# Optimization experiments

Hardware: AMD Instinct MI355X
Metric: run time of the kernel (lower is better)

Reference implementation:

```python
import jax, jax.numpy as jnp
import numpy as np

N_NODES = 10000
N_EDGES = 50000
NUM_GENES = 1000
HEADS = 8
DIMS_IN = [256, 448 * 8, 384 * 8, 256 * 8]
DIMS_OUT = [448, 384, 256, NUM_GENES]
HEADS_L = [8, 8, 8, 1]


def _leaky_relu(x):
    return jnp.where(x >= 0, x, 0.2 * x)


def gat_conv(x, src, dst, n, W, a_src, a_dst, b, heads, c):
    # W: [heads*c, f_in]; a_src/a_dst: [heads, c]; b: [heads*c]
    h = (x @ W.T).reshape(n, heads, c)                      # [N,H,C]
    al_s = jnp.einsum('nhc,hc->nh', h, a_src)               # [N,H]
    al_d = jnp.einsum('nhc,hc->nh', h, a_dst)
    e = _leaky_relu(al_s[src] + al_d[dst])                  # [E,H]
    # segment softmax over incoming edges of each dst node
    m = jax.ops.segment_max(e, dst, num_segments=n)
    e = jnp.exp(e - m[dst])
    s = jax.ops.segment_sum(e, dst, num_segments=n)
    alpha = e / (s[dst] + 1e-16)
    out = jax.ops.segment_sum(h[src] * alpha[:, :, None], dst, num_segments=n)
    return out.reshape(n, heads * c) + b


def graph_ln(x, w, b):
    # PyG LayerNorm mode='graph': normalize over all node features of the graph
    mu = x.mean()
    var = ((x - mu) ** 2).mean()
    return (x - mu) * jax.lax.rsqrt(var + 1e-5) * w + b


def setup_inputs() -> dict:
    key = jax.random.key(0)
    ks = jax.random.split(key, 32)
    inp = {
        'x': jax.random.normal(ks[0], (N_NODES, DIMS_IN[0]), dtype=jnp.float32),
        'edge_index': jax.random.randint(ks[1], (2, N_EDGES), 0, N_NODES, dtype=jnp.int32),
    }
    ki = 2
    for li in range(4):
        h, c, fin = HEADS_L[li], DIMS_OUT[li], DIMS_IN[li]
        inp[f'W{li+1}'] = jax.random.normal(ks[ki], (h * c, fin), dtype=jnp.float32) * (fin ** -0.5); ki += 1
        inp[f'a_src{li+1}'] = jax.random.normal(ks[ki], (h, c), dtype=jnp.float32) * 0.1; ki += 1
        inp[f'a_dst{li+1}'] = jax.random.normal(ks[ki], (h, c), dtype=jnp.float32) * 0.1; ki += 1
        inp[f'b{li+1}'] = jnp.zeros((h * c,), dtype=jnp.float32)
        if li < 3:
            inp[f'ln{li+1}_w'] = jnp.ones((h * c,), dtype=jnp.float32)
            inp[f'ln{li+1}_b'] = jnp.zeros((h * c,), dtype=jnp.float32)
    return inp


def reference(x, edge_index,
              W1, a_src1, a_dst1, b1, ln1_w, ln1_b,
              W2, a_src2, a_dst2, b2, ln2_w, ln2_b,
              W3, a_src3, a_dst3, b3, ln3_w, ln3_b,
              W4, a_src4, a_dst4, b4):
    n = x.shape[0]
    loops = jnp.arange(n, dtype=edge_index.dtype)
    src = jnp.concatenate([edge_index[0], loops])  # add_self_loops=True (PyG default)
    dst = jnp.concatenate([edge_index[1], loops])
    h = jax.nn.relu(gat_conv(x, src, dst, n, W1, a_src1, a_dst1, b1, 8, 448))
    h = graph_ln(h, ln1_w, ln1_b)
    h = jax.nn.relu(gat_conv(h, src, dst, n, W2, a_src2, a_dst2, b2, 8, 384))
    h = graph_ln(h, ln2_w, ln2_b)
    h = jax.nn.relu(gat_conv(h, src, dst, n, W3, a_src3, a_dst3, b3, 8, 256))
    h = graph_ln(h, ln3_w, ln3_b)
    out = gat_conv(h, src, dst, n, W4, a_src4, a_dst4, b4, 1, NUM_GENES)
    return out
```

## Files before the change

kernel.cpp:

```cpp
#include <hip/hip_runtime.h>

typedef _Float16 h8 __attribute__((ext_vector_type(8)));
typedef _Float16 h4 __attribute__((ext_vector_type(4)));
typedef __attribute__((ext_vector_type(4))) float facc4;

__device__ __forceinline__ void gload16(const void* g, void* l) {
  __builtin_amdgcn_global_load_lds((const __attribute__((address_space(1))) void*)g,
                                   (__attribute__((address_space(3))) void*)l, 16, 0, 0);
}

__global__ void f2h_k(const float* __restrict__ in, unsigned short* __restrict__ out, int n4) {
  int i = blockIdx.x * 256 + threadIdx.x;
  int stride = gridDim.x * 256;
  for (; i < n4; i += stride) {
    float4 v = ((const float4*)in)[i];
    h4 o;
    o[0] = (_Float16)v.x; o[1] = (_Float16)v.y; o[2] = (_Float16)v.z; o[3] = (_Float16)v.w;
    ((h4*)out)[i] = o;
  }
}

__global__ __launch_bounds__(512, 2) void gemm_f16(
    const unsigned short* __restrict__ A, const unsigned short* __restrict__ B,
    unsigned short* __restrict__ Hout,
    float* __restrict__ als, float* __restrict__ ald,
    const float* __restrict__ a_src, const float* __restrict__ a_dst,
    int M, int Nn, int K, int C, int H, int gx, int nwg) {
  __shared__ __align__(16) unsigned short lds[3 * 16384];
  const int tid = threadIdx.x, lane = tid & 63, wv = tid >> 6;

  int lin = blockIdx.x;
  int q = nwg >> 3, r = nwg & 7;
  int xcd = lin & 7, idx = lin >> 3;
  int swz = (xcd < r) ? (xcd * (q + 1) + idx) : (r * (q + 1) + (xcd - r) * q + idx);
  const int bx = swz % gx, by = swz / gx;
  const int brow = by * 256, bcol = bx * 256;
  const int wr = wv >> 2, wc = wv & 3;

  const int l4 = lane >> 2;
  const int srcslot = ((lane & 3) ^ ((lane >> 3) & 3)) * 8;
  int ar0 = brow + wv * 16 + l4;        if (ar0 > M - 1)  ar0 = M - 1;
  int ar1 = brow + wv * 16 + 128 + l4;  if (ar1 > M - 1)  ar1 = M - 1;
  int br0 = bcol + wv * 16 + l4;        if (br0 > Nn - 1) br0 = Nn - 1;
  int br1 = bcol + wv * 16 + 128 + l4;  if (br1 > Nn - 1) br1 = Nn - 1;
  const unsigned short* pa0 = A + (size_t)ar0 * K + srcslot;
  const unsigned short* pa1 = A + (size_t)ar1 * K + srcslot;
  const unsigned short* pb0 = B + (size_t)br0 * K + srcslot;
  const unsigned short* pb1 = B + (size_t)br1 * K + srcslot;
  const int d0 = wv * 512, d1 = wv * 512 + 4096;

  const int rsl = ((lane >> 4) ^ (((lane & 15) >> 1) & 3)) * 8;
  const int baseA = (wr * 128 + (lane & 15)) * 32 + rsl;
  const int baseB = 8192 + (wc * 64 + (lane & 15)) * 32 + rsl;

  facc4 acc[8][4] = {};
  const int nt = K >> 5;

  auto STAGE = [&](int kt, int buf) {
    unsigned short* Lq = &lds[buf * 16384];
    const int kb = kt * 32;
    gload16(pa0 + kb, Lq + d0);
    gload16(pa1 + kb, Lq + d1);
    gload16(pb0 + kb, Lq + 8192 + d0);
    gload16(pb1 + kb, Lq + 8192 + d1);
  };

  STAGE(0, 0);
  STAGE(1, 1);
  asm volatile("s_waitcnt vmcnt(4)" ::: "memory");
  __builtin_amdgcn_s_barrier();
  asm volatile("" ::: "memory");

  int cb = 0, sb = 2;
  for (int kt = 0; kt < nt; ++kt) {
    if (kt + 2 < nt) STAGE(kt + 2, sb);
    const unsigned short* Lq = &lds[cb * 16384];
    h8 af[8], bf[4];
#pragma unroll
    for (int m = 0; m < 8; ++m) af[m] = *(const h8*)(Lq + baseA + m * 512);
#pragma unroll
    for (int n = 0; n < 4; ++n) bf[n] = *(const h8*)(Lq + baseB + n * 512);
    __builtin_amdgcn_s_setprio(1);
#pragma unroll
    for (int m = 0; m < 8; ++m)
#pragma unroll
      for (int n = 0; n < 4; ++n)
        acc[m][n] = __builtin_amdgcn_mfma_f32_16x16x32_f16(af[m], bf[n], acc[m][n], 0, 0, 0);
    __builtin_amdgcn_s_setprio(0);
    if (kt + 2 < nt) asm volatile("s_waitcnt vmcnt(4)" ::: "memory");
    else             asm volatile("s_waitcnt vmcnt(0)" ::: "memory");
    __builtin_amdgcn_s_barrier();
    asm volatile("" ::: "memory");
    cb = (cb == 2) ? 0 : cb + 1;
    sb = (sb == 2) ? 0 : sb + 1;
  }

  const int rbase = brow + wr * 128 + ((lane >> 4) << 2);
  const int cbase = bcol + wc * 64 + (lane & 15);

  float asv[4], adv[4];
#pragma unroll
  for (int n = 0; n < 4; ++n) {
    int col = cbase + n * 16;
    bool ok = col < Nn;
    asv[n] = ok ? a_src[col] : 0.f;
    adv[n] = ok ? a_dst[col] : 0.f;
  }
  const int hh = (bcol + wc * 64) / C;
#pragma unroll
  for (int m = 0; m < 8; ++m)
#pragma unroll
    for (int r2 = 0; r2 < 4; ++r2) {
      float s1 = 0.f, s2 = 0.f;
#pragma unroll
      for (int n = 0; n < 4; ++n) { float v = acc[m][n][r2]; s1 += v * asv[n]; s2 += v * adv[n]; }
#pragma unroll
      for (int mm = 1; mm < 16; mm <<= 1) { s1 += __shfl_xor(s1, mm); s2 += __shfl_xor(s2, mm); }
      int row = rbase + m * 16 + r2;
      if ((lane & 15) == 0 && row < M) {
        atomicAdd(&als[row * H + hh], s1);
        atomicAdd(&ald[row * H + hh], s2);
      }
    }

#pragma unroll
  for (int m = 0; m < 8; ++m)
#pragma unroll
    for (int n = 0; n < 4; ++n) {
      int col = cbase + n * 16;
      if (col >= Nn) continue;
#pragma unroll
      for (int r2 = 0; r2 < 4; ++r2) {
        int row = rbase + m * 16 + r2;
        if (row < M) {
          _Float16 hv = (_Float16)acc[m][n][r2];
          Hout[(size_t)row * Nn + col] = *(unsigned short*)&hv;
        }
      }
    }
}

__global__ __launch_bounds__(512, 2) void gemm_f16_hd(
    const unsigned short* __restrict__ Aall, const unsigned short* __restrict__ Ball,
    unsigned short* __restrict__ Xout, const float* __restrict__ bias,
    float* __restrict__ lnsums, int M, int K, int Fo, int Ch, int gx, int nwg) {
  __shared__ __align__(16) unsigned short lds[3 * 16384];
  const int tid = threadIdx.x, lane = tid & 63, wv = tid >> 6;
  const int head = blockIdx.y;
  const unsigned short* A = Aall + (size_t)head * M * K;
  const unsigned short* B = Ball + (size_t)head * Ch * K;

  int lin = blockIdx.x;
  int q = nwg >> 3, r = nwg & 7;
  int xcd = lin & 7, idx = lin >> 3;
  int swz = (xcd < r) ? (xcd * (q + 1) + idx) : (r * (q + 1) + (xcd - r) * q + idx);
  const int bx = swz % gx, by = swz / gx;
  const int brow = by * 256, bcol = bx * 256;
  const int wr = wv >> 2, wc = wv & 3;

  const int l4 = lane >> 2;
  const int srcslot = ((lane & 3) ^ ((lane >> 3) & 3)) * 8;
  int ar0 = brow + wv * 16 + l4;        if (ar0 > M - 1)  ar0 = M - 1;
  int ar1 = brow + wv * 16 + 128 + l4;  if (ar1 > M - 1)  ar1 = M - 1;
  int br0 = bcol + wv * 16 + l4;        if (br0 > Ch - 1) br0 = Ch - 1;
  int br1 = bcol + wv * 16 + 128 + l4;  if (br1 > Ch - 1) br1 = Ch - 1;
  const unsigned short* pa0 = A + (size_t)ar0 * K + srcslot;
  const unsigned short* pa1 = A + (size_t)ar1 * K + srcslot;
  const unsigned short* pb0 = B + (size_t)br0 * K + srcslot;
  const unsigned short* pb1 = B + (size_t)br1 * K + srcslot;
  const int d0 = wv * 512, d1 = wv * 512 + 4096;

  const int rsl = ((lane >> 4) ^ (((lane & 15) >> 1) & 3)) * 8;
  const int baseA = (wr * 128 + (lane & 15)) * 32 + rsl;
  const int baseB = 8192 + (wc * 64 + (lane & 15)) * 32 + rsl;

  facc4 acc[8][4] = {};
  const int nt = K >> 5;

  auto STAGE = [&](int kt, int buf) {
    unsigned short* Lq = &lds[buf * 16384];
    const int kb = kt * 32;
    gload16(pa0 + kb, Lq + d0);
    gload16(pa1 + kb, Lq + d1);
    gload16(pb0 + kb, Lq + 8192 + d0);
    gload16(pb1 + kb, Lq + 8192 + d1);
  };

  STAGE(0, 0);
  STAGE(1, 1);
  asm volatile("s_waitcnt vmcnt(4)" ::: "memory");
  __builtin_amdgcn_s_barrier();
  asm volatile("" ::: "memory");

  int cb = 0, sb = 2;
  for (int kt = 0; kt < nt; ++kt) {
    if (kt + 2 < nt) STAGE(kt + 2, sb);
    const unsigned short* Lq = &lds[cb * 16384];
    h8 af[8], bf[4];
#pragma unroll
    for (int m = 0; m < 8; ++m) af[m] = *(const h8*)(Lq + baseA + m * 512);
#pragma unroll
    for (int n = 0; n < 4; ++n) bf[n] = *(const h8*)(Lq + baseB + n * 512);
    __builtin_amdgcn_s_setprio(1);
#pragma unroll
    for (int m = 0; m < 8; ++m)
#pragma unroll
      for (int n = 0; n < 4; ++n)
        acc[m][n] = __builtin_amdgcn_mfma_f32_16x16x32_f16(af[m], bf[n], acc[m][n], 0, 0, 0);
    __builtin_amdgcn_s_setprio(0);
    if (kt + 2 < nt) asm volatile("s_waitcnt vmcnt(4)" ::: "memory");
    else             asm volatile("s_waitcnt vmcnt(0)" ::: "memory");
    __builtin_amdgcn_s_barrier();
    asm volatile("" ::: "memory");
    cb = (cb == 2) ? 0 : cb + 1;
    sb = (sb == 2) ? 0 : sb + 1;
  }

  const int rbase = brow + wr * 128 + ((lane >> 4) << 2);
  const int cbase = bcol + wc * 64 + (lane & 15);
  float s1 = 0.f, s2 = 0.f;
#pragma unroll
  for (int n = 0; n < 4; ++n) {
    int col_l = cbase + n * 16;
    if (col_l >= Ch) continue;
    int col_g = head * Ch + col_l;
    float bv = bias[col_g];
#pragma unroll
    for (int m = 0; m < 8; ++m)
#pragma unroll
      for (int r2 = 0; r2 < 4; ++r2) {
        int row = rbase + m * 16 + r2;
        if (row < M) {
          float v = acc[m][n][r2] + bv;
          _Float16 hv = (_Float16)v;
          Xout[(size_t)row * Fo + col_g] = *(unsigned short*)&hv;
          float rv = v > 0.f ? v : 0.f;
          s1 += rv; s2 += rv * rv;
        }
      }
  }
#pragma unroll
  for (int m = 32; m; m >>= 1) { s1 += __shfl_down(s1, m); s2 += __shfl_down(s2, m); }
  __shared__ float r1s[8], r2s[8];
  if (lane == 0) { r1s[wv] = s1; r2s[wv] = s2; }
  __syncthreads();
  if (tid == 0) {
    float t1 = 0.f, t2 = 0.f;
#pragma unroll
    for (int w = 0; w < 8; ++w) { t1 += r1s[w]; t2 += r2s[w]; }
    atomicAdd(&lnsums[0], t1);
    atomicAdd(&lnsums[1], t2);
  }
}

__global__ void attw_k(const float* __restrict__ W, const float* __restrict__ as_,
                       const float* __restrict__ ad_, float* __restrict__ ws,
                       float* __restrict__ wd, int C, int K) {
  int t = blockIdx.x * 256 + threadIdx.x;
  int h = t / K, k = t % K;
  float s1 = 0.f, s2 = 0.f;
  for (int c = 0; c < C; ++c) {
    float w = W[(size_t)(h * C + c) * K + k];
    s1 += as_[h * C + c] * w;
    s2 += ad_[h * C + c] * w;
  }
  ws[t] = s1; wd[t] = s2;
}

__global__ __launch_bounds__(256) void logits_x_k(
    const float* __restrict__ x, const float* __restrict__ ws, const float* __restrict__ wd,
    float* __restrict__ als, float* __restrict__ ald, int n) {
  __shared__ float sws[2048], swd[2048];
  for (int i = threadIdx.x; i < 2048; i += 256) { sws[i] = ws[i]; swd[i] = wd[i]; }
  __syncthreads();
  int node = blockIdx.x * 4 + (threadIdx.x >> 6);
  int lane = threadIdx.x & 63;
  if (node >= n) return;
  const float* xp = x + (size_t)node * 256;
  float s1[8] = {}, s2[8] = {};
  for (int k = lane; k < 256; k += 64) {
    float xv = xp[k];
#pragma unroll
    for (int h = 0; h < 8; ++h) { s1[h] += xv * sws[h * 256 + k]; s2[h] += xv * swd[h * 256 + k]; }
  }
#pragma unroll
  for (int m = 32; m; m >>= 1)
#pragma unroll
    for (int h = 0; h < 8; ++h) { s1[h] += __shfl_down(s1[h], m); s2[h] += __shfl_down(s2[h], m); }
  if (lane == 0) {
#pragma unroll
    for (int h = 0; h < 8; ++h) { als[node * 8 + h] = s1[h]; ald[node * 8 + h] = s2[h]; }
  }
}

__global__ __launch_bounds__(256) void aggregate_x_k(
    const unsigned short* __restrict__ x16,
    const float* __restrict__ als, const float* __restrict__ ald,
    const int* __restrict__ rowptr, const int* __restrict__ esrc,
    unsigned short* __restrict__ aggx, int n) {
  const int node = blockIdx.x, tid = threadIdx.x;
  int beg = rowptr[node];
  int deg = rowptr[node + 1] - beg;
  if (deg > 64) deg = 64;
  __shared__ int   s_src[64];
  __shared__ float s_al[64][8];
  __shared__ float s_inv[8];
  __shared__ unsigned short s_x[64][256];
  float aldv[8];
#pragma unroll
  for (int h = 0; h < 8; ++h) aldv[h] = ald[node * 8 + h];
  for (int d = tid; d < deg; d += 256) {
    int s = esrc[beg + d];
    s_src[d] = s;
#pragma unroll
    for (int h = 0; h < 8; ++h) {
      float v = als[s * 8 + h] + aldv[h];
      s_al[d][h] = (v >= 0.f) ? v : 0.2f * v;
    }
  }
  __syncthreads();
  if (tid < 8) {
    float m = -1e30f;
    for (int d = 0; d < deg; ++d) m = fmaxf(m, s_al[d][tid]);
    float s = 0.f;
    for (int d = 0; d < deg; ++d) { float p = __expf(s_al[d][tid] - m); s_al[d][tid] = p; s += p; }
    s_inv[tid] = 1.f / (s + 1e-16f);
  }
  for (int c = tid; c < deg * 32; c += 256) {
    int d = c >> 5, q = c & 31;
    ((h8*)s_x[d])[q] = ((const h8*)(x16 + (size_t)s_src[d] * 256))[q];
  }
  __syncthreads();
  const int h = tid >> 5, k8 = tid & 31;
  float a[8] = {};
  for (int d = 0; d < deg; ++d) {
    float al = s_al[d][h] * s_inv[h];
    h8 xv = ((const h8*)s_x[d])[k8];
#pragma unroll
    for (int j = 0; j < 8; ++j) a[j] = fmaf(al, (float)xv[j], a[j]);
  }
  h8 o;
#pragma unroll
  for (int j = 0; j < 8; ++j) o[j] = (_Float16)a[j];
  *(h8*)(aggx + ((size_t)h * n + node) * 256 + k8 * 8) = o;
}

__global__ void count_deg_k(const int* __restrict__ ei, int* __restrict__ deg, int Ereal, int Etot) {
  int e = blockIdx.x * 256 + threadIdx.x;
  if (e >= Etot) return;
  int dst = (e < Ereal) ? ei[Ereal + e] : (e - Ereal);
  atomicAdd(&deg[dst], 1);
}

__global__ void scan_k(const int* __restrict__ deg, int* __restrict__ rowptr, int n) {
  __shared__ int sums[1024];
  int t = threadIdx.x;
  int base = t * 10;
  int loc[10]; int s = 0;
#pragma unroll
  for (int i = 0; i < 10; ++i) { int idx = base + i; int d = (idx < n) ? deg[idx] : 0; loc[i] = s; s += d; }
  sums[t] = s;
  __syncthreads();
  for (int off = 1; off < 1024; off <<= 1) {
    int add = (t >= off) ? sums[t - off] : 0;
    __syncthreads();
    sums[t] += add;
    __syncthreads();
  }
  int excl = sums[t] - s;
#pragma unroll
  for (int i = 0; i < 10; ++i) { int idx = base + i; if (idx < n) rowptr[idx] = excl + loc[i]; }
  if (t == 1023) rowptr[n] = sums[1023];
}

__global__ void scatter_k(const int* __restrict__ ei, const int* __restrict__ rowptr,
                          int* __restrict__ fill, int* __restrict__ esrc,
                          int Ereal, int Etot) {
  int e = blockIdx.x * 256 + threadIdx.x;
  if (e >= Etot) return;
  int src = (e < Ereal) ? ei[e] : (e - Ereal);
  int dst = (e < Ereal) ? ei[Ereal + e] : (e - Ereal);
  int pos = rowptr[dst] + atomicAdd(&fill[dst], 1);
  esrc[pos] = src;
}

template <int H, bool FP32OUT, bool STATS>
__global__ __launch_bounds__(256) void aggregate_k(
    const unsigned short* __restrict__ hfp,
    const float* __restrict__ als, const float* __restrict__ ald,
    const int* __restrict__ rowptr, const int* __restrict__ esrc,
    const float* __restrict__ bias, void* __restrict__ outv,
    float* __restrict__ lnsums, int C, int F) {
  const int node = blockIdx.x;
  const int tid = threadIdx.x;
  int beg = rowptr[node];
  int deg = rowptr[node + 1] - beg;
  if (deg > 128) deg = 128;
  __shared__ int   s_src[128];
  __shared__ float s_p[128][H];
  __shared__ float s_inv[H];
  float aldv[H];
#pragma unroll
  for (int h = 0; h < H; ++h) aldv[h] = ald[node * H + h];
  for (int d = tid; d < deg; d += 256) {
    int s = esrc[beg + d];
    s_src[d] = s;
#pragma unroll
    for (int h = 0; h < H; ++h) {
      float v = als[s * H + h] + aldv[h];
      s_p[d][h] = (v >= 0.f) ? v : 0.2f * v;
    }
  }
  __syncthreads();
  if (tid < H) {
    float m = -1e30f;
    for (int d = 0; d < deg; ++d) m = fmaxf(m, s_p[d][tid]);
    float s = 0.f;
    for (int d = 0; d < deg; ++d) { float p = __expf(s_p[d][tid] - m); s_p[d][tid] = p; s += p; }
    s_inv[tid] = 1.f / (s + 1e-16f);
  }
  __syncthreads();

  float s1 = 0.f, s2 = 0.f;
  const int F8 = F >> 3;
  for (int c8 = tid; c8 < F8; c8 += 256) {
    int f0 = c8 * 8;
    int h = f0 / C;
    float a[8];
    float4 b0 = *(const float4*)(bias + f0);
    float4 b1 = *(const float4*)(bias + f0 + 4);
    a[0] = b0.x; a[1] = b0.y; a[2] = b0.z; a[3] = b0.w;
    a[4] = b1.x; a[5] = b1.y; a[6] = b1.z; a[7] = b1.w;
    for (int d = 0; d < deg; ++d) {
      float al = s_p[d][h] * s_inv[h];
      h8 hv = *(const h8*)(hfp + (size_t)s_src[d] * F + f0);
#pragma unroll
      for (int j = 0; j < 8; ++j) a[j] = fmaf(al, (float)hv[j], a[j]);
    }
    size_t i = (size_t)node * F + f0;
    if (FP32OUT) {
      float4 o0 = {a[0], a[1], a[2], a[3]};
      float4 o1 = {a[4], a[5], a[6], a[7]};
      *(float4*)((float*)outv + i) = o0;
      *(float4*)((float*)outv + i + 4) = o1;
    } else {
      h8 o;
#pragma unroll
      for (int j = 0; j < 8; ++j) o[j] = (_Float16)a[j];
      *(h8*)((unsigned short*)outv + i) = o;
    }
    if (STATS) {
#pragma unroll
      for (int j = 0; j < 8; ++j) { float v = a[j] > 0.f ? a[j] : 0.f; s1 += v; s2 += v * v; }
    }
  }
  if (STATS) {
#pragma unroll
    for (int m = 32; m; m >>= 1) { s1 += __shfl_down(s1, m); s2 += __shfl_down(s2, m); }
    __shared__ float r1[4], r2[4];
    if ((tid & 63) == 0) { r1[tid >> 6] = s1; r2[tid >> 6] = s2; }
    __syncthreads();
    if (tid == 0) {
      atomicAdd(&lnsums[0], r1[0] + r1[1] + r1[2] + r1[3]);
      atomicAdd(&lnsums[1], r2[0] + r2[1] + r2[2] + r2[3]);
    }
  }
}

__global__ void ln_apply_k(unsigned short* __restrict__ x, const float* __restrict__ sums,
                           const float* __restrict__ w, const float* __restrict__ b,
                           int total8, int F8, float inv_count) {
  int i8 = blockIdx.x * 256 + threadIdx.x;
  if (i8 >= total8) return;
  float mu = sums[0] * inv_count;
  float var = sums[1] * inv_count - mu * mu;
  float istd = rsqrtf(var + 1e-5f);
  int f0 = (i8 % F8) * 8;
  h8 hv = *(h8*)(x + (size_t)i8 * 8);
  float4 w0 = *(const float4*)(w + f0), w1 = *(const float4*)(w + f0 + 4);
  float4 b0 = *(const float4*)(b + f0), b1 = *(const float4*)(b + f0 + 4);
  float wv[8] = {w0.x, w0.y, w0.z, w0.w, w1.x, w1.y, w1.z, w1.w};
  float bv[8] = {b0.x, b0.y, b0.z, b0.w, b1.x, b1.y, b1.z, b1.w};
  h8 o;
#pragma unroll
  for (int j = 0; j < 8; ++j) {
    float v = (float)hv[j]; v = v > 0.f ? v : 0.f;
    o[j] = (_Float16)((v - mu) * istd * wv[j] + bv[j]);
  }
  *(h8*)(x + (size_t)i8 * 8) = o;
}

extern "C" void kernel_launch(void* const* d_in, const int* in_sizes, int n_in,
                              void* d_out, int out_size, void* d_ws, size_t ws_size,
                              hipStream_t stream) {
  const int N = 10000, Ereal = 50000, Etot = 60000;
  const float* x  = (const float*)d_in[0];
  const int*   ei = (const int*)d_in[1];
  const float* W[4]    = {(const float*)d_in[2],  (const float*)d_in[8],  (const float*)d_in[14], (const float*)d_in[20]};
  const float* asrc[4] = {(const float*)d_in[3],  (const float*)d_in[9],  (const float*)d_in[15], (const float*)d_in[21]};
  const float* adst[4] = {(const float*)d_in[4],  (const float*)d_in[10], (const float*)d_in[16], (const float*)d_in[22]};
  const float* bias[4] = {(const float*)d_in[5],  (const float*)d_in[11], (const float*)d_in[17], (const float*)d_in[23]};
  const float* lnw[3]  = {(const float*)d_in[6],  (const float*)d_in[12], (const float*)d_in[18]};
  const float* lnb[3]  = {(const float*)d_in[7],  (const float*)d_in[13], (const float*)d_in[19]};

  const int fin[4]  = {256, 3584, 3072, 2048};
  const int fout[4] = {3584, 3072, 2048, 1000};
  const int CH[4]   = {448, 384, 256, 1000};

  size_t off = 0;
  char* base = (char*)d_ws;
  auto alloc = [&](size_t bytes) -> void* {
    void* p = base + off;
    off += (bytes + 255) & ~(size_t)255;
    return p;
  };
  unsigned short* xh  = (unsigned short*)alloc((size_t)N * 3584 * 2);
  unsigned short* hh  = (unsigned short*)alloc((size_t)N * 3584 * 2);
  unsigned short* wh  = (unsigned short*)alloc((size_t)3072 * 3584 * 2);
  float*          alsA   = (float*)alloc((size_t)4 * N * 8 * 4);
  float*          aldA   = (float*)alloc((size_t)4 * N * 8 * 4);
  int*            deg    = (int*)alloc((size_t)N * 4);
  int*            fill   = (int*)alloc((size_t)N * 4);
  int*            rowptr = (int*)alloc((size_t)(N + 1) * 4);
  int*            esrc   = (int*)alloc((size_t)Etot * 4);
  float*          lnsums = (float*)alloc(256);
  float*          wsrc   = (float*)alloc((size_t)8 * 256 * 4);
  float*          wdst   = (float*)alloc((size_t)8 * 256 * 4);

  auto cdiv = [](int a, int b) { return (a + b - 1) / b; };

  hipMemsetAsync(deg, 0, (size_t)N * 4, stream);
  hipMemsetAsync(fill, 0, (size_t)N * 4, stream);
  hipMemsetAsync(alsA, 0, (size_t)4 * N * 8 * 4 * 2, stream);
  count_deg_k<<<cdiv(Etot, 256), 256, 0, stream>>>(ei, deg, Ereal, Etot);
  scan_k<<<1, 1024, 0, stream>>>(deg, rowptr, N);
  scatter_k<<<cdiv(Etot, 256), 256, 0, stream>>>(ei, rowptr, fill, esrc, Ereal, Etot);

  {
    int n4 = (N * fin[0]) / 4;
    f2h_k<<<min(2048, cdiv(n4, 256)), 256, 0, stream>>>(x, xh, n4);
  }

  {
    float* als = alsA;
    float* ald = aldA;
    attw_k<<<8, 256, 0, stream>>>(W[0], asrc[0], adst[0], wsrc, wdst, 448, 256);
    logits_x_k<<<cdiv(N, 4), 256, 0, stream>>>(x, wsrc, wdst, als, ald, N);
    {
      int n4 = (3584 * 256) / 4;
      f2h_k<<<min(2048, cdiv(n4, 256)), 256, 0, stream>>>(W[0], wh, n4);
    }
    aggregate_x_k<<<N, 256, 0, stream>>>(xh, als, ald, rowptr, esrc, hh, N);
    hipMemsetAsync(lnsums, 0, 8, stream);
    gemm_f16_hd<<<dim3(80, 8), 512, 0, stream>>>(hh, wh, xh, bias[0], lnsums,
                                                 N, 256, 3584, 448, 2, 80);
    int F8 = 3584 >> 3;
    ln_apply_k<<<cdiv(N * F8, 256), 256, 0, stream>>>(xh, lnsums, lnw[0], lnb[0],
                                                      N * F8, F8, 1.0f / (float)(N * 3584));
  }

  for (int l = 1; l < 4; ++l) {
    const int K = fin[l], Fo = fout[l], C = CH[l];
    const int H = (l == 3) ? 1 : 8;
    float* als = alsA + (size_t)l * N * 8;
    float* ald = aldA + (size_t)l * N * 8;

    {
      int n4 = (Fo * K) / 4;
      f2h_k<<<min(2048, cdiv(n4, 256)), 256, 0, stream>>>(W[l], wh, n4);
    }

    {
      int gx = cdiv(Fo, 256), gy = cdiv(N, 256);
      int nwg = gx * gy;
      gemm_f16<<<nwg, 512, 0, stream>>>(xh, wh, hh, als, ald, asrc[l], adst[l],
                                        N, Fo, K, C, H, gx, nwg);
    }

    if (l < 3) {
      hipMemsetAsync(lnsums, 0, 8, stream);
      aggregate_k<8, false, true><<<N, 256, 0, stream>>>(hh, als, ald, rowptr, esrc,
                                                         bias[l], xh, lnsums, C, Fo);
      int F8 = Fo >> 3;
      int total8 = N * F8;
      ln_apply_k<<<cdiv(total8, 256), 256, 0, stream>>>(xh, lnsums, lnw[l], lnb[l],
                                                        total8, F8, 1.0f / (float)(N * Fo));
    } else {
      aggregate_k<1, true, false><<<N, 256, 0, stream>>>(hh, als, ald, rowptr, esrc,
                                                         bias[l], d_out, nullptr, C, Fo);
    }
  }
}
```

Before: 1.504 ms.

## Fold graph LayerNorm into next layer's weights and drop ln_apply passes

Removes the separate ln_apply kernels. The activation is now stored post-ReLU, and the LayerNorm scale (istd*w) is folded into the fp16 weight conversion, with a per-output constant (W·(b - mu*istd*w)) computed in the same kernel and added to the GEMM accumulator. This saves a full read-modify-write pass over the large N×F activation per layer, plus some memsets. In exchange, the weight-conversion kernel does more per-element work and a reduction, and scaling the weights before fp16 rounding changes numerics, since the activation is no longer centred before the matmul.

```diff
diff --git a/kernel.cpp b/kernel.cpp
--- a/kernel.cpp
+++ b/kernel.cpp
@@ -20,11 +20,42 @@
   }
 }
 
+__global__ __launch_bounds__(256) void w2h_fold_k(
+    const float* __restrict__ W, const float* __restrict__ lnw, const float* __restrict__ lnb,
+    const float* __restrict__ sums, float inv_count,
+    unsigned short* __restrict__ wh, float* __restrict__ cvec, int K) {
+  const int o = blockIdx.x, tid = threadIdx.x;
+  float mu = sums[0] * inv_count;
+  float var = sums[1] * inv_count - mu * mu;
+  float istd = rsqrtf(var + 1e-5f);
+  const float* wrow = W + (size_t)o * K;
+  float dot = 0.f;
+  for (int k4 = tid; k4 < (K >> 2); k4 += 256) {
+    float4 wv = ((const float4*)wrow)[k4];
+    float4 gw = ((const float4*)lnw)[k4];
+    float4 gb = ((const float4*)lnb)[k4];
+    float sx = istd * gw.x, sy = istd * gw.y, sz = istd * gw.z, sw = istd * gw.w;
+    h4 oq;
+    oq[0] = (_Float16)(wv.x * sx); oq[1] = (_Float16)(wv.y * sy);
+    oq[2] = (_Float16)(wv.z * sz); oq[3] = (_Float16)(wv.w * sw);
+    ((h4*)(wh + (size_t)o * K))[k4] = oq;
+    dot += wv.x * (gb.x - mu * sx) + wv.y * (gb.y - mu * sy)
+         + wv.z * (gb.z - mu * sz) + wv.w * (gb.w - mu * sw);
+  }
+#pragma unroll
+  for (int m = 32; m; m >>= 1) dot += __shfl_down(dot, m);
+  __shared__ float r[4];
+  if ((tid & 63) == 0) r[tid >> 6] = dot;
+  __syncthreads();
+  if (tid == 0) cvec[o] = r[0] + r[1] + r[2] + r[3];
+}
+
 __global__ __launch_bounds__(512, 2) void gemm_f16(
     const unsigned short* __restrict__ A, const unsigned short* __restrict__ B,
     unsigned short* __restrict__ Hout,
     float* __restrict__ als, float* __restrict__ ald,
     const float* __restrict__ a_src, const float* __restrict__ a_dst,
+    const float* __restrict__ cvec,
     int M, int Nn, int K, int C, int H, int gx, int nwg) {
   __shared__ __align__(16) unsigned short lds[3 * 16384];
   const int tid = threadIdx.x, lane = tid & 63, wv = tid >> 6;
@@ -98,6 +129,16 @@
   const int rbase = brow + wr * 128 + ((lane >> 4) << 2);
   const int cbase = bcol + wc * 64 + (lane & 15);
 
+#pragma unroll
+  for (int n = 0; n < 4; ++n) {
+    int col = cbase + n * 16;
+    float cadd = (col < Nn) ? cvec[col] : 0.f;
+#pragma unroll
+    for (int m = 0; m < 8; ++m)
+#pragma unroll
+      for (int r2 = 0; r2 < 4; ++r2) acc[m][n][r2] += cadd;
+  }
+
   float asv[4], adv[4];
 #pragma unroll
   for (int n = 0; n < 4; ++n) {
@@ -232,9 +273,9 @@
         int row = rbase + m * 16 + r2;
         if (row < M) {
           float v = acc[m][n][r2] + bv;
-          _Float16 hv = (_Float16)v;
+          float rv = v > 0.f ? v : 0.f;
+          _Float16 hv = (_Float16)rv;
           Xout[(size_t)row * Fo + col_g] = *(unsigned short*)&hv;
-          float rv = v > 0.f ? v : 0.f;
           s1 += rv; s2 += rv * rv;
         }
       }
@@ -327,8 +368,8 @@
     s_inv[tid] = 1.f / (s + 1e-16f);
   }
   for (int c = tid; c < deg * 32; c += 256) {
-    int d = c >> 5, q = c & 31;
-    ((h8*)s_x[d])[q] = ((const h8*)(x16 + (size_t)s_src[d] * 256))[q];
+    int d = c >> 5, q2 = c & 31;
+    ((h8*)s_x[d])[q2] = ((const h8*)(x16 + (size_t)s_src[d] * 256))[q2];
   }
   __syncthreads();
   const int h = tid >> 5, k8 = tid & 31;
@@ -437,6 +478,10 @@
 #pragma unroll
       for (int j = 0; j < 8; ++j) a[j] = fmaf(al, (float)hv[j], a[j]);
     }
+    if (STATS) {
+#pragma unroll
+      for (int j = 0; j < 8; ++j) { float v = a[j] > 0.f ? a[j] : 0.f; a[j] = v; s1 += v; s2 += v * v; }
+    }
     size_t i = (size_t)node * F + f0;
     if (FP32OUT) {
       float4 o0 = {a[0], a[1], a[2], a[3]};
@@ -449,10 +494,6 @@
       for (int j = 0; j < 8; ++j) o[j] = (_Float16)a[j];
       *(h8*)((unsigned short*)outv + i) = o;
     }
-    if (STATS) {
-#pragma unroll
-      for (int j = 0; j < 8; ++j) { float v = a[j] > 0.f ? a[j] : 0.f; s1 += v; s2 += v * v; }
-    }
   }
   if (STATS) {
 #pragma unroll
@@ -465,29 +506,6 @@
       atomicAdd(&lnsums[1], r2[0] + r2[1] + r2[2] + r2[3]);
     }
   }
-}
-
-__global__ void ln_apply_k(unsigned short* __restrict__ x, const float* __restrict__ sums,
-                           const float* __restrict__ w, const float* __restrict__ b,
-                           int total8, int F8, float inv_count) {
-  int i8 = blockIdx.x * 256 + threadIdx.x;
-  if (i8 >= total8) return;
-  float mu = sums[0] * inv_count;
-  float var = sums[1] * inv_count - mu * mu;
-  float istd = rsqrtf(var + 1e-5f);
-  int f0 = (i8 % F8) * 8;
-  h8 hv = *(h8*)(x + (size_t)i8 * 8);
-  float4 w0 = *(const float4*)(w + f0), w1 = *(const float4*)(w + f0 + 4);
-  float4 b0 = *(const float4*)(b + f0), b1 = *(const float4*)(b + f0 + 4);
-  float wv[8] = {w0.x, w0.y, w0.z, w0.w, w1.x, w1.y, w1.z, w1.w};
-  float bv[8] = {b0.x, b0.y, b0.z, b0.w, b1.x, b1.y, b1.z, b1.w};
-  h8 o;
-#pragma unroll
-  for (int j = 0; j < 8; ++j) {
-    float v = (float)hv[j]; v = v > 0.f ? v : 0.f;
-    o[j] = (_Float16)((v - mu) * istd * wv[j] + bv[j]);
-  }
-  *(h8*)(x + (size_t)i8 * 8) = o;
 }
 
 extern "C" void kernel_launch(void* const* d_in, const int* in_sizes, int n_in,
@@ -519,19 +537,20 @@
   unsigned short* wh  = (unsigned short*)alloc((size_t)3072 * 3584 * 2);
   float*          alsA   = (float*)alloc((size_t)4 * N * 8 * 4);
   float*          aldA   = (float*)alloc((size_t)4 * N * 8 * 4);
+  float*          lnsA   = (float*)alloc(256);
   int*            deg    = (int*)alloc((size_t)N * 4);
   int*            fill   = (int*)alloc((size_t)N * 4);
   int*            rowptr = (int*)alloc((size_t)(N + 1) * 4);
   int*            esrc   = (int*)alloc((size_t)Etot * 4);
-  float*          lnsums = (float*)alloc(256);
   float*          wsrc   = (float*)alloc((size_t)8 * 256 * 4);
   float*          wdst   = (float*)alloc((size_t)8 * 256 * 4);
+  float*          cvec   = (float*)alloc((size_t)3072 * 4);
 
   auto cdiv = [](int a, int b) { return (a + b - 1) / b; };
 
   hipMemsetAsync(deg, 0, (size_t)N * 4, stream);
   hipMemsetAsync(fill, 0, (size_t)N * 4, stream);
-  hipMemsetAsync(alsA, 0, (size_t)4 * N * 8 * 4 * 2, stream);
+  hipMemsetAsync(alsA, 0, (size_t)4 * N * 8 * 4 * 2 + 256, stream);
   count_deg_k<<<cdiv(Etot, 256), 256, 0, stream>>>(ei, deg, Ereal, Etot);
   scan_k<<<1, 1024, 0, stream>>>(deg, rowptr, N);
   scatter_k<<<cdiv(Etot, 256), 256, 0, stream>>>(ei, rowptr, fill, esrc, Ereal, Etot);
@@ -551,12 +570,8 @@
       f2h_k<<<min(2048, cdiv(n4, 256)), 256, 0, stream>>>(W[0], wh, n4);
     }
     aggregate_x_k<<<N, 256, 0, stream>>>(xh, als, ald, rowptr, esrc, hh, N);
-    hipMemsetAsync(lnsums, 0, 8, stream);
-    gemm_f16_hd<<<dim3(80, 8), 512, 0, stream>>>(hh, wh, xh, bias[0], lnsums,
+    gemm_f16_hd<<<dim3(80, 8), 512, 0, stream>>>(hh, wh, xh, bias[0], lnsA,
                                                  N, 256, 3584, 448, 2, 80);
-    int F8 = 3584 >> 3;
-    ln_apply_k<<<cdiv(N * F8, 256), 256, 0, stream>>>(xh, lnsums, lnw[0], lnb[0],
-                                                      N * F8, F8, 1.0f / (float)(N * 3584));
   }
 
   for (int l = 1; l < 4; ++l) {
@@ -565,26 +580,19 @@
     float* als = alsA + (size_t)l * N * 8;
     float* ald = aldA + (size_t)l * N * 8;
 
-    {
-      int n4 = (Fo * K) / 4;
-      f2h_k<<<min(2048, cdiv(n4, 256)), 256, 0, stream>>>(W[l], wh, n4);
-    }
+    w2h_fold_k<<<Fo, 256, 0, stream>>>(W[l], lnw[l - 1], lnb[l - 1], lnsA + (l - 1) * 2,
+                                       1.0f / (float)(N * fin[l]), wh, cvec, K);
 
     {
       int gx = cdiv(Fo, 256), gy = cdiv(N, 256);
       int nwg = gx * gy;
-      gemm_f16<<<nwg, 512, 0, stream>>>(xh, wh, hh, als, ald, asrc[l], adst[l],
+      gemm_f16<<<nwg, 512, 0, stream>>>(xh, wh, hh, als, ald, asrc[l], adst[l], cvec,
                                         N, Fo, K, C, H, gx, nwg);
     }
 
     if (l < 3) {
-      hipMemsetAsync(lnsums, 0, 8, stream);
       aggregate_k<8, false, true><<<N, 256, 0, stream>>>(hh, als, ald, rowptr, esrc,
-                                                         bias[l], xh, lnsums, C, Fo);
-      int F8 = Fo >> 3;
-      int total8 = N * F8;
-      ln_apply_k<<<cdiv(total8, 256), 256, 0, stream>>>(xh, lnsums, lnw[l], lnb[l],
-                                                        total8, F8, 1.0f / (float)(N * Fo));
+                                                         bias[l], xh, lnsA + l * 2, C, Fo);
     } else {
       aggregate_k<1, true, false><<<N, 256, 0, stream>>>(hh, als, ald, rowptr, esrc,
                                                          bias[l], d_out, nullptr, C, Fo);
```

Measured after the change: 1.426 ms. 5.2% less time.
